# Performance work log

Hardware: AMD Instinct MI355X
Metric: run time of the kernel (lower is better)

## Reference

```python
import jax, jax.numpy as jnp
import numpy as np

# Model dims (match init_kwargs)
HID = 1024   # hidden_size
H   = 16     # num_heads
DK  = 64     # head_dim (key)
DV  = 128    # head value dim = int(head_dim * expand_v)
VAL = H * DV # value_dim = 2048
CONV = 4     # short conv kernel size
EPS = 1e-6
NORM_EPS = 1e-5


def _causal_conv_silu(x, w):
    # x: [B,T,C], w: [C,K] depthwise causal conv, no bias, silu activation
    T = x.shape[1]
    K = w.shape[1]
    xp = jnp.pad(x, ((0, 0), (K - 1, 0), (0, 0)))
    y = sum(xp[:, i:i + T, :] * w[:, i] for i in range(K))
    return jax.nn.silu(y)


def setup_inputs() -> dict:
    key = jax.random.key(0)
    ks = jax.random.split(key, 16)
    s = 0.02
    rn = lambda k, sh: jax.random.normal(k, sh, jnp.float32)
    return {
        'hidden_states': rn(ks[0], (1, 2048, HID)),
        'norm_w': jnp.ones((HID,), jnp.float32),
        'q_w': rn(ks[1], (H * DK, HID)) * s,
        'k_w': rn(ks[2], (H * DK, HID)) * s,
        'v_w': rn(ks[3], (VAL, HID)) * s,
        'a_w': rn(ks[4], (H, HID)) * s,
        'b_w': rn(ks[5], (H, HID)) * s,
        'g_w': rn(ks[6], (VAL, HID)) * s,
        'dt_bias': jax.random.uniform(ks[7], (H,), jnp.float32, -2.0, 0.0),
        'A_log': jnp.log(jax.random.uniform(ks[8], (H,), jnp.float32, 1.0, 8.0)),
        'conv_q_w': rn(ks[9], (H * DK, CONV)) * 0.2,
        'conv_k_w': rn(ks[10], (H * DK, CONV)) * 0.2,
        'conv_v_w': rn(ks[11], (VAL, CONV)) * 0.2,
        'o_norm_w': jnp.ones((DV,), jnp.float32),
        'o_proj_w': rn(ks[12], (HID, VAL)) * s,
        'out_proj_w': rn(ks[13], (HID, HID)) * s,
    }


def reference(hidden_states, norm_w, q_w, k_w, v_w, a_w, b_w, g_w, dt_bias,
              A_log, conv_q_w, conv_k_w, conv_v_w, o_norm_w, o_proj_w, out_proj_w):
    B, T, D = hidden_states.shape
    # RMSNorm
    x = hidden_states * jax.lax.rsqrt(
        jnp.mean(hidden_states * hidden_states, -1, keepdims=True) + EPS) * norm_w

    # projections + causal depthwise short conv + silu
    q = _causal_conv_silu(x @ q_w.T, conv_q_w).reshape(B, T, H, DK)
    k = _causal_conv_silu(x @ k_w.T, conv_k_w).reshape(B, T, H, DK)
    v = _causal_conv_silu(x @ v_w.T, conv_v_w).reshape(B, T, H, DV)

    beta = jax.nn.sigmoid(x @ b_w.T)                       # [B,T,H]
    g = -jnp.exp(A_log) * jax.nn.softplus(x @ a_w.T + dt_bias)  # [B,T,H] log-decay

    # rank-1 DC removal on keys: (I - 1 1^T / DK) k, i.e. subtract per-head mean
    k = k - jnp.mean(k, -1, keepdims=True)

    # L2 normalize q, k along head dim; scale q
    q = q * jax.lax.rsqrt(jnp.sum(q * q, -1, keepdims=True) + EPS)
    k = k * jax.lax.rsqrt(jnp.sum(k * k, -1, keepdims=True) + EPS)
    q = q * (DK ** -0.5)

    # gated delta-rule recurrence over time (time-major scan)
    qT = q.transpose(1, 0, 2, 3)
    kT = k.transpose(1, 0, 2, 3)
    vT = v.transpose(1, 0, 2, 3)
    bT = beta.transpose(1, 0, 2)
    gT = g.transpose(1, 0, 2)

    def step(S, inp):
        qt, kt, vt, bt, gt = inp              # S: [B,H,DK,DV]
        S = S * jnp.exp(gt)[..., None, None]
        v_new = (vt - jnp.einsum('bhk,bhkv->bhv', kt, S)) * bt[..., None]
        S = S + jnp.einsum('bhk,bhv->bhkv', kt, v_new)
        o = jnp.einsum('bhk,bhkv->bhv', qt, S)
        return S, o

    S0 = jnp.zeros((B, H, DK, DV), x.dtype)
    _, oT = jax.lax.scan(step, S0, (qT, kT, vT, bT, gT))
    o = oT.transpose(1, 0, 2, 3)                           # [B,T,H,DV]

    # gated RMSNorm on output heads
    gate = (x @ g_w.T).reshape(B, T, H, DV)
    o = o * jax.lax.rsqrt(jnp.mean(o * o, -1, keepdims=True) + NORM_EPS) * o_norm_w
    o = o * jax.nn.silu(gate)

    o = o.reshape(B, T, VAL) @ o_proj_w.T                  # [B,T,HID]
    return o @ out_proj_w.T
```

## Files before the change

kernel.cpp:

```cpp
#include <hip/hip_runtime.h>
#include <math.h>

#define S72 72

typedef __bf16 bf16;
typedef __bf16 bf16x8 __attribute__((ext_vector_type(8)));
typedef __bf16 bf16x4v __attribute__((ext_vector_type(4)));
typedef __bf16 bf16x2v __attribute__((ext_vector_type(2)));
typedef float f32x4 __attribute__((ext_vector_type(4)));

__device__ __forceinline__ float wredsum(float v) {
#pragma unroll
  for (int off = 32; off > 0; off >>= 1) v += __shfl_xor(v, off, 64);
  return v;
}
__device__ __forceinline__ float sigmoidf_(float x) { return 1.f / (1.f + __expf(-x)); }

__device__ __forceinline__ int sxy(int row, int col) {
  return (row << 6) + ((((col >> 3) ^ (row & 7)) << 3) | (col & 7));
}
__device__ __forceinline__ int sx8(int row, int chunk) {
  return (row << 6) + ((chunk ^ (row & 7)) << 3);
}

__global__ __launch_bounds__(256) void k_pre(const float* __restrict__ h,
    const float* __restrict__ nw, const float* __restrict__ aw,
    const float* __restrict__ bw, const float* __restrict__ dtb,
    const float* __restrict__ alog, bf16* __restrict__ xb,
    float* __restrict__ graw, float* __restrict__ btb,
    const float* __restrict__ qw, const float* __restrict__ kw,
    const float* __restrict__ vw, const float* __restrict__ gw,
    const float* __restrict__ opw, const float* __restrict__ ow,
    bf16* qwb, bf16* kwb, bf16* vwb, bf16* gwb, bf16* opwb, bf16* owb) {
  __shared__ float red[4];
  __shared__ __align__(16) float xs[1024];
  int tid = threadIdx.x;
  if (blockIdx.x >= 2048) {
    long cb = blockIdx.x - 2048;
    for (long u = cb*256 + tid; u < 2359296; u += 4608l*256) {
      const float* src; bf16* dst; long l;
      if      (u <  262144) { src=qw;  dst=qwb;  l=u; }
      else if (u <  524288) { src=kw;  dst=kwb;  l=u-262144; }
      else if (u < 1048576) { src=vw;  dst=vwb;  l=u-524288; }
      else if (u < 1572864) { src=gw;  dst=gwb;  l=u-1048576; }
      else if (u < 2097152) { src=opw; dst=opwb; l=u-1572864; }
      else                  { src=ow;  dst=owb;  l=u-2097152; }
      float4 s = *(const float4*)(src + l*4);
      bf16x4v b; b[0]=(bf16)s.x; b[1]=(bf16)s.y; b[2]=(bf16)s.z; b[3]=(bf16)s.w;
      *(bf16x4v*)(dst + l*4) = b;
    }
    return;
  }
  int t = blockIdx.x;
  float4 hv = *(const float4*)(h + (size_t)t*1024 + tid*4);
  float ss = hv.x*hv.x + hv.y*hv.y + hv.z*hv.z + hv.w*hv.w;
  float wsum = wredsum(ss);
  if ((tid & 63) == 0) red[tid >> 6] = wsum;
  __syncthreads();
  float tot = red[0] + red[1] + red[2] + red[3];
  float rs = rsqrtf(tot * (1.f/1024.f) + 1e-6f);
  float4 w4 = *(const float4*)(nw + tid*4);
  float4 y;
  y.x = hv.x*rs*w4.x; y.y = hv.y*rs*w4.y; y.z = hv.z*rs*w4.z; y.w = hv.w*rs*w4.w;
  *(float4*)(xs + tid*4) = y;
  bf16x4v b; b[0]=(bf16)y.x; b[1]=(bf16)y.y; b[2]=(bf16)y.z; b[3]=(bf16)y.w;
  *(bf16x4v*)(xb + (size_t)t*1024 + tid*4) = b;
  __syncthreads();
  int wave = tid >> 6, lane = tid & 63;
  const float4* x4 = (const float4*)xs;
#pragma unroll
  for (int hi = 0; hi < 4; ++hi) {
    int hh = wave*4 + hi;
    float sa = 0.f, sb = 0.f;
#pragma unroll
    for (int i = 0; i < 4; ++i) {
      float4 xv = x4[i*64 + lane];
      float4 av = *(const float4*)(aw + hh*1024 + i*256 + lane*4);
      float4 bv = *(const float4*)(bw + hh*1024 + i*256 + lane*4);
      sa += xv.x*av.x + xv.y*av.y + xv.z*av.z + xv.w*av.w;
      sb += xv.x*bv.x + xv.y*bv.y + xv.z*bv.z + xv.w*bv.w;
    }
    sa = wredsum(sa); sb = wredsum(sb);
    if (lane == 0) {
      float ap = sa + dtb[hh];
      float sp = (ap > 20.f) ? ap : log1pf(expf(ap));
      graw[t*16 + hh] = -expf(alog[hh]) * sp;
      btb[t*16 + hh] = 1.f / (1.f + expf(-sb));
    }
  }
}

template <typename OutT>
__device__ __forceinline__ void gemm_body(const bf16* __restrict__ A,
    const bf16* __restrict__ B, OutT* __restrict__ C, int N, int K, int m0, int n0) {
  __shared__ bf16 As[2][128*32];
  __shared__ bf16 Bs[2][128*32];
  const int tid = threadIdx.x, lane = tid & 63, wave = tid >> 6;
  const int wm = (wave >> 1) * 64, wn = (wave & 1) * 64;
  const int srow = wave*16 + (lane >> 2);
  const int swl = (((lane & 3) ^ ((lane >> 3) & 3))) * 8;
  const int sdst = (lane & 3) * 8;
  const int quad = lane >> 4, l16 = lane & 15;
  const int sw = (l16 >> 1) & 3;
  f32x4 acc[4][4] = {};
  const int nk = K >> 5;
#pragma unroll
  for (int i = 0; i < 2; ++i) {
    int r = i*64 + srow;
    __builtin_amdgcn_global_load_lds(
      (__attribute__((address_space(1))) void*)(A + (size_t)(m0 + r)*K + swl),
      (__attribute__((address_space(3))) void*)(&As[0][r*32 + sdst]), 16, 0, 0);
    __builtin_amdgcn_global_load_lds(
      (__attribute__((address_space(1))) void*)(B + (size_t)(n0 + r)*K + swl),
      (__attribute__((address_space(3))) void*)(&Bs[0][r*32 + sdst]), 16, 0, 0);
  }
  for (int kt = 0; kt < nk; ++kt) {
    const int cur = kt & 1;
    __syncthreads();
    bf16x8 af[4], bfr[4];
#pragma unroll
    for (int mt = 0; mt < 4; ++mt)
      af[mt] = *(const bf16x8*)(&As[cur][(wm + mt*16 + l16)*32 + (quad ^ sw)*8]);
#pragma unroll
    for (int nt = 0; nt < 4; ++nt)
      bfr[nt] = *(const bf16x8*)(&Bs[cur][(wn + nt*16 + l16)*32 + (quad ^ sw)*8]);
    if (kt + 1 < nk) {
      int k0 = (kt + 1) << 5;
#pragma unroll
      for (int i = 0; i < 2; ++i) {
        int r = i*64 + srow;
        __builtin_amdgcn_global_load_lds(
          (__attribute__((address_space(1))) void*)(A + (size_t)(m0 + r)*K + k0 + swl),
          (__attribute__((address_space(3))) void*)(&As[cur^1][r*32 + sdst]), 16, 0, 0);
        __builtin_amdgcn_global_load_lds(
          (__attribute__((address_space(1))) void*)(B + (size_t)(n0 + r)*K + k0 + swl),
          (__attribute__((address_space(3))) void*)(&Bs[cur^1][r*32 + sdst]), 16, 0, 0);
      }
    }
#pragma unroll
    for (int mt = 0; mt < 4; ++mt)
#pragma unroll
      for (int nt = 0; nt < 4; ++nt)
        acc[mt][nt] = __builtin_amdgcn_mfma_f32_16x16x32_bf16(af[mt], bfr[nt], acc[mt][nt], 0, 0, 0);
  }
#pragma unroll
  for (int mt = 0; mt < 4; ++mt)
#pragma unroll
    for (int nt = 0; nt < 4; ++nt)
#pragma unroll
      for (int r = 0; r < 4; ++r) {
        int row = m0 + wm + mt*16 + quad*4 + r;
        int col = n0 + wn + nt*16 + l16;
        C[(size_t)row*N + col] = (OutT)acc[mt][nt][r];
      }
}

__global__ __launch_bounds__(256) void k_gemm_proj(const bf16* __restrict__ A,
    const bf16* __restrict__ qwb, const bf16* __restrict__ kwb,
    const bf16* __restrict__ vwb, const bf16* __restrict__ gwb,
    bf16* __restrict__ qpre, bf16* __restrict__ kpre,
    bf16* __restrict__ vpre, bf16* __restrict__ gpre) {
  int bx = blockIdx.x;
  const bf16* B; bf16* C; int N, xt;
  if      (bx <  8) { B = qwb; C = qpre; N = 1024; xt = bx; }
  else if (bx < 16) { B = kwb; C = kpre; N = 1024; xt = bx - 8; }
  else if (bx < 32) { B = vwb; C = vpre; N = 2048; xt = bx - 16; }
  else              { B = gwb; C = gpre; N = 2048; xt = bx - 32; }
  gemm_body<bf16>(A, B, C, N, 1024, blockIdx.y*128, xt*128);
}

template <typename OutT>
__global__ __launch_bounds__(256) void k_gemm_bt64(const bf16* __restrict__ A,
    const bf16* __restrict__ B, OutT* __restrict__ C, int N, int K) {
  __shared__ bf16 As[2][128*32];
  __shared__ bf16 Bs[2][64*32];
  const int tid = threadIdx.x, lane = tid & 63, wave = tid >> 6;
  const int wm = wave * 32;
  const int srow = wave*16 + (lane >> 2);
  const int swl = (((lane & 3) ^ ((lane >> 3) & 3))) * 8;
  const int sdst = (lane & 3) * 8;
  const int quad = lane >> 4, l16 = lane & 15;
  const int sw = (l16 >> 1) & 3;
  const int m0 = blockIdx.y * 128, n0 = blockIdx.x * 64;
  f32x4 acc[2][4] = {};
  const int nk = K >> 5;
#pragma unroll
  for (int i = 0; i < 2; ++i) {
    int r = i*64 + srow;
    __builtin_amdgcn_global_load_lds(
      (__attribute__((address_space(1))) void*)(A + (size_t)(m0 + r)*K + swl),
      (__attribute__((address_space(3))) void*)(&As[0][r*32 + sdst]), 16, 0, 0);
  }
  __builtin_amdgcn_global_load_lds(
    (__attribute__((address_space(1))) void*)(B + (size_t)(n0 + srow)*K + swl),
    (__attribute__((address_space(3))) void*)(&Bs[0][srow*32 + sdst]), 16, 0, 0);
  for (int kt = 0; kt < nk; ++kt) {
    const int cur = kt & 1;
    __syncthreads();
    bf16x8 af[2], bfr[4];
#pragma unroll
    for (int mt = 0; mt < 2; ++mt)
      af[mt] = *(const bf16x8*)(&As[cur][(wm + mt*16 + l16)*32 + (quad ^ sw)*8]);
#pragma unroll
    for (int nt = 0; nt < 4; ++nt)
      bfr[nt] = *(const bf16x8*)(&Bs[cur][(nt*16 + l16)*32 + (quad ^ sw)*8]);
    if (kt + 1 < nk) {
      int k0 = (kt + 1) << 5;
#pragma unroll
      for (int i = 0; i < 2; ++i) {
        int r = i*64 + srow;
        __builtin_amdgcn_global_load_lds(
          (__attribute__((address_space(1))) void*)(A + (size_t)(m0 + r)*K + k0 + swl),
          (__attribute__((address_space(3))) void*)(&As[cur^1][r*32 + sdst]), 16, 0, 0);
      }
      __builtin_amdgcn_global_load_lds(
        (__attribute__((address_space(1))) void*)(B + (size_t)(n0 + srow)*K + k0 + swl),
        (__attribute__((address_space(3))) void*)(&Bs[cur^1][srow*32 + sdst]), 16, 0, 0);
    }
#pragma unroll
    for (int mt = 0; mt < 2; ++mt)
#pragma unroll
      for (int nt = 0; nt < 4; ++nt)
        acc[mt][nt] = __builtin_amdgcn_mfma_f32_16x16x32_bf16(af[mt], bfr[nt], acc[mt][nt], 0, 0, 0);
  }
#pragma unroll
  for (int mt = 0; mt < 2; ++mt)
#pragma unroll
    for (int nt = 0; nt < 4; ++nt)
#pragma unroll
      for (int r = 0; r < 4; ++r) {
        int row = m0 + wm + mt*16 + quad*4 + r;
        int col = n0 + nt*16 + l16;
        C[(size_t)row*N + col] = (OutT)acc[mt][nt][r];
      }
}

template<int NT>
__device__ __forceinline__ void mm_band(const bf16* A_lds, const bf16* B_lds,
    int w16, int cb, int l16, int quad, f32x4* acc) {
#pragma unroll
  for (int n = 0; n < NT; ++n) { acc[n][0]=0.f; acc[n][1]=0.f; acc[n][2]=0.f; acc[n][3]=0.f; }
#pragma unroll
  for (int kt = 0; kt < 2; ++kt) {
    bf16x8 af = *(const bf16x8*)(A_lds + sx8(w16 + l16, kt*4 + quad));
#pragma unroll
    for (int n = 0; n < NT; ++n) {
      bf16x8 bf = *(const bf16x8*)(B_lds + sx8(cb + n*16 + l16, kt*4 + quad));
      acc[n] = __builtin_amdgcn_mfma_f32_16x16x32_bf16(af, bf, acc[n], 0, 0, 0);
    }
  }
}

__global__ __launch_bounds__(512, 4) void k_prepass(
    const bf16* __restrict__ qpre, const bf16* __restrict__ kpre,
    const bf16* __restrict__ vpre, const float* __restrict__ cqw,
    const float* __restrict__ ckw, const float* __restrict__ cvw,
    const float* __restrict__ graw, const float* __restrict__ beta,
    bf16* __restrict__ EF, float* __restrict__ dSl, float* __restrict__ obuf) {
  const int bx = blockIdx.x, c = bx >> 4, h = bx & 15, tid = threadIdx.x;
  const int t0 = c * 64;
  const int wave = tid >> 6, lane = tid & 63, l16 = lane & 15, quad = lane >> 4;
  const int w16 = (wave >> 1) * 16;
  const int chh = wave & 1;
  const int r0 = wave * 8;

  __shared__ bf16 SM[36864];
  __shared__ float bs[64], bts_s[64], es[64], gms[64];
  bf16* Kr    = SM;
  bf16* powR0 = SM + 4096;
  bf16* prod0 = SM + 8192;
  bf16* T2T   = SM + 12288;
  bf16* powT0 = SM + 16384;
  bf16* powR1 = SM + 20480;
  bf16* powT1 = SM + 24576;
  bf16* prod1 = SM + 28672;
  bf16* qbf   = SM + 32768;
  bf16* VT   = SM;
  bf16* VlT  = SM + 8192;
  bf16* KT   = powT0;
  bf16* KbT  = powR1;
  bf16* Pm   = powT1;
  bf16* WR   = prod0;
  bf16* Mrow = prod1;

  if (tid < 64) {
    float g = graw[(size_t)(t0 + tid)*16 + h];
    float b = g;
#pragma unroll
    for (int off = 1; off < 64; off <<= 1) {
      float p = __shfl_up(b, off, 64);
      if (tid >= off) b += p;
    }
    bs[tid] = b;
    bts_s[tid] = beta[(size_t)(t0 + tid)*16 + h];
    float b63 = __shfl(b, 63, 64);
    es[tid] = __expf(b63 - b);
    gms[tid] = __expf(b);
  }

  float kreg[8], vreg[16];
  {
    float4 wq  = *(const float4*)(cqw + (h*64 + lane)*4);
    float4 wk  = *(const float4*)(ckw + (h*64 + lane)*4);
    float4 wv0 = *(const float4*)(cvw + (h*128 + lane)*4);
    float4 wv1 = *(const float4*)(cvw + (h*128 + 64 + lane)*4);
    float qtv[11], ktv[11], vtv0[11], vtv1[11];
#pragma unroll
    for (int j = 0; j < 11; ++j) {
      int tg = t0 + r0 + j - 3;
      bool ok = tg >= 0;
      qtv[j]  = ok ? (float)qpre[(size_t)tg*1024 + h*64 + lane] : 0.f;
      ktv[j]  = ok ? (float)kpre[(size_t)tg*1024 + h*64 + lane] : 0.f;
      vtv0[j] = ok ? (float)vpre[(size_t)tg*2048 + h*128 + lane] : 0.f;
      vtv1[j] = ok ? (float)vpre[(size_t)tg*2048 + h*128 + 64 + lane] : 0.f;
    }
#pragma unroll
    for (int rr = 0; rr < 8; ++rr) {
      float y = qtv[rr]*wq.x + qtv[rr+1]*wq.y + qtv[rr+2]*wq.z + qtv[rr+3]*wq.w;
      y = y * sigmoidf_(y);
      float ssq = wredsum(y*y);
      y *= rsqrtf(ssq + 1e-6f) * 0.125f;
      qbf[sxy(r0+rr, lane)] = (bf16)y;
    }
#pragma unroll
    for (int rr = 0; rr < 8; ++rr) {
      float y = ktv[rr]*wk.x + ktv[rr+1]*wk.y + ktv[rr+2]*wk.z + ktv[rr+3]*wk.w;
      y = y * sigmoidf_(y);
      float s1 = y, s2 = y*y;
#pragma unroll
      for (int off = 32; off > 0; off >>= 1) {
        s1 += __shfl_xor(s1, off, 64);
        s2 += __shfl_xor(s2, off, 64);
      }
      float m = s1 * (1.f/64.f);
      float ssq = s2 - s1*m;
      y -= m;
      y *= rsqrtf(ssq + 1e-6f);
      kreg[rr] = y;
      Kr[sxy(r0+rr, lane)] = (bf16)y;
    }
#pragma unroll
    for (int rr = 0; rr < 8; ++rr) {
      float y0 = vtv0[rr]*wv0.x + vtv0[rr+1]*wv0.y + vtv0[rr+2]*wv0.z + vtv0[rr+3]*wv0.w;
      float y1 = vtv1[rr]*wv1.x + vtv1[rr+1]*wv1.y + vtv1[rr+2]*wv1.z + vtv1[rr+3]*wv1.w;
      vreg[rr]   = y0 * sigmoidf_(y0);
      vreg[8+rr] = y1 * sigmoidf_(y1);
    }
  }
  __syncthreads();

  {
    f32x4 acc[2];
    mm_band<2>(Kr, Kr, w16, chh*32, l16, quad, acc);
#pragma unroll
    for (int n = 0; n < 2; ++n) {
      int col = chh*32 + n*16 + l16;
      bf16x4v tv;
#pragma unroll
      for (int r = 0; r < 4; ++r) {
        int row = w16 + quad*4 + r;
        float nv = 0.f;
        if (row > col) nv = -bts_s[row] * __expf(bs[row] - bs[col]) * acc[n][r];
        bf16 nb = (bf16)nv;
        powR0[sxy(row, col)] = nb;
        tv[r] = nb;
        prod0[sxy(row, col)] = (row == col) ? (bf16)1.f : nb;
      }
      *(bf16x4v*)(powT0 + sxy(col, w16 + quad*4)) = tv;
    }
  }
  __syncthreads();

  int pc = 0, rc = 0;
#pragma unroll 1
  for (int i = 1; i <= 5; ++i) {
    bf16* sqA = pc ? powR1 : powR0;
    bf16* sqB = pc ? powT1 : powT0;
    bf16* sqRo = pc ? powR0 : powR1;
    bf16* sqTo = pc ? powT0 : powT1;
    {
      f32x4 acc[2];
      mm_band<2>(sqA, sqB, w16, chh*32, l16, quad, acc);
#pragma unroll
      for (int n = 0; n < 2; ++n) {
        int col = chh*32 + n*16 + l16;
        bf16x4v tv;
#pragma unroll
        for (int r = 0; r < 4; ++r) {
          int row = w16 + quad*4 + r;
          bf16 vb = (bf16)acc[n][r];
          sqRo[sxy(row, col)] = vb;
          tv[r] = vb;
        }
        *(bf16x4v*)(sqTo + sxy(col, w16 + quad*4)) = tv;
      }
    }
    __syncthreads();
    bf16* prA = rc ? prod1 : prod0;
    bf16* prO = rc ? prod0 : prod1;
    {
      f32x4 acc[2];
      mm_band<2>(prA, sqTo, w16, chh*32, l16, quad, acc);
#pragma unroll
      for (int n = 0; n < 2; ++n) {
        int col = chh*32 + n*16 + l16;
        bf16x4v tv;
#pragma unroll
        for (int r = 0; r < 4; ++r) {
          int row = w16 + quad*4 + r;
          float val = acc[n][r] + (float)prA[sxy(row, col)];
          prO[sxy(row, col)] = (bf16)val;
          tv[r] = (bf16)(val * bts_s[col] * gms[col]);
        }
        if (i == 5) *(bf16x4v*)(T2T + sxy(col, w16 + quad*4)) = tv;
      }
    }
    __syncthreads();
    pc ^= 1; rc ^= 1;
  }

#pragma unroll
  for (int rr = 0; rr < 8; ++rr) {
    KT[sxy(lane, r0+rr)]  = (bf16)kreg[rr];
    KbT[sxy(lane, r0+rr)] = (bf16)(kreg[rr] * es[r0+rr]);
  }
  {
    f32x4 acc[2];
#pragma unroll
    for (int n = 0; n < 2; ++n) { acc[n][0]=0.f; acc[n][1]=0.f; acc[n][2]=0.f; acc[n][3]=0.f; }
#pragma unroll
    for (int kt = 0; kt < 2; ++kt) {
      bf16x8 af = *(const bf16x8*)(qbf + sx8(w16 + l16, kt*4 + quad));
#pragma unroll
      for (int n = 0; n < 2; ++n) {
        bf16x8 bf = *(const bf16x8*)(Kr + sx8(chh*32 + n*16 + l16, kt*4 + quad));
        acc[n] = __builtin_amdgcn_mfma_f32_16x16x32_bf16(af, bf, acc[n], 0, 0, 0);
      }
    }
#pragma unroll
    for (int n = 0; n < 2; ++n) {
      int col = chh*32 + n*16 + l16;
#pragma unroll
      for (int r = 0; r < 4; ++r) {
        int row = w16 + quad*4 + r;
        float pv = (row >= col) ? __expf(bs[row] - bs[col]) * acc[n][r] : 0.f;
        Pm[sxy(row, col)] = (bf16)pv;
      }
    }
  }
  __syncthreads();

  {
    f32x4 acc[2];
    mm_band<2>(KbT, T2T, w16, chh*32, l16, quad, acc);
#pragma unroll
    for (int n = 0; n < 2; ++n) {
      int col = chh*32 + n*16 + l16;
#pragma unroll
      for (int r = 0; r < 4; ++r)
        WR[sxy(w16 + quad*4 + r, col)] = (bf16)acc[n][r];
    }
  }
#pragma unroll
  for (int hf = 0; hf < 2; ++hf)
#pragma unroll
    for (int rr = 0; rr < 8; ++rr)
      VT[sxy(hf*64 + lane, r0+rr)] = (bf16)(bts_s[r0+rr] * vreg[hf*8+rr]);
  __syncthreads();
  {
    f32x4 acc[2];
    mm_band<2>(WR, KT, w16, chh*32, l16, quad, acc);
    float gC = gms[63];
    size_t eb = (size_t)bx * 13824;
#pragma unroll
    for (int n = 0; n < 2; ++n) {
      int col = chh*32 + n*16 + l16;
#pragma unroll
      for (int r = 0; r < 4; ++r) {
        int row = w16 + quad*4 + r;
        float ev = ((row == col) ? gC : 0.f) - acc[n][r];
        bf16 eh = (bf16)ev;
        EF[eb + row*S72 + col] = eh;
        EF[eb + 4608 + row*S72 + col] = (bf16)(ev - (float)eh);
      }
    }
  }
  __syncthreads();
  {
    f32x4 acc[2];
    mm_band<2>(Pm, T2T, w16, chh*32, l16, quad, acc);
#pragma unroll
    for (int n = 0; n < 2; ++n) {
      int col = chh*32 + n*16 + l16;
#pragma unroll
      for (int r = 0; r < 4; ++r)
        WR[sxy(w16 + quad*4 + r, col)] = (bf16)acc[n][r];
    }
  }
  __syncthreads();
  {
    f32x4 acc[2];
    mm_band<2>(WR, KT, w16, chh*32, l16, quad, acc);
    size_t eb = (size_t)bx * 13824;
#pragma unroll
    for (int n = 0; n < 2; ++n) {
      int col = chh*32 + n*16 + l16;
#pragma unroll
      for (int r = 0; r < 4; ++r) {
        int row = w16 + quad*4 + r;
        float qv = (float)qbf[sxy(row, col)];
        EF[eb + 9216 + row*S72 + col] = (bf16)(gms[row]*qv - acc[n][r]);
      }
    }
  }
  __syncthreads();
  {
    f32x4 acc[4];
    mm_band<4>(Mrow, VT, w16, chh*64, l16, quad, acc);
#pragma unroll
    for (int n = 0; n < 4; ++n) {
      int col = chh*64 + n*16 + l16;
      bf16x4v tv;
#pragma unroll
      for (int r = 0; r < 4; ++r) tv[r] = (bf16)acc[n][r];
      *(bf16x4v*)(VlT + sxy(col, w16 + quad*4)) = tv;
    }
  }
  __syncthreads();
  {
    f32x4 acc[4];
    mm_band<4>(KbT, VlT, w16, chh*64, l16, quad, acc);
#pragma unroll
    for (int n = 0; n < 4; ++n) {
      int col = chh*64 + n*16 + l16;
#pragma unroll
      for (int r = 0; r < 4; ++r)
        dSl[(size_t)bx*8192 + (size_t)(w16 + quad*4 + r)*128 + col] = acc[n][r];
    }
  }
  {
    f32x4 acc[4];
    mm_band<4>(Pm, VlT, w16, chh*64, l16, quad, acc);
#pragma unroll
    for (int n = 0; n < 4; ++n) {
      int col = chh*64 + n*16 + l16;
#pragma unroll
      for (int r = 0; r < 4; ++r)
        obuf[(size_t)(t0 + w16 + quad*4 + r)*2048 + h*128 + col] = acc[n][r];
    }
  }
}

#define SEQ_LOAD(Cn, EHx, ELx, FFx, DSx)                                        \
  {                                                                             \
    const bf16* base_ = EF + (size_t)((Cn)*16 + h)*13824 + arow;                \
    _Pragma("unroll")                                                           \
    for (int kt = 0; kt < 2; ++kt) {                                            \
      EHx[kt] = *(const bf16x8*)(base_ + kt*32);                                \
      ELx[kt] = *(const bf16x8*)(base_ + 4608 + kt*32);                         \
      FFx[kt] = *(const bf16x8*)(base_ + 9216 + kt*32);                         \
    }                                                                           \
    const float* db_ = dSl + (size_t)((Cn)*16 + h)*8192 + drow;                 \
    _Pragma("unroll")                                                           \
    for (int nt = 0; nt < 2; ++nt)                                              \
      _Pragma("unroll")                                                         \
      for (int r = 0; r < 4; ++r)                                               \
        DSx[nt*4+r] = db_[(size_t)r*128 + nt*16];                               \
  }

#define SEQ_STEP(Cc, EHc, ELc, FFc, DSc, EHn, ELn, FFn, DSn, SRC, DST)          \
  {                                                                             \
    bf16x8 bh[2][2], bl[2][2];                                                  \
    _Pragma("unroll")                                                           \
    for (int nt = 0; nt < 2; ++nt)                                              \
      _Pragma("unroll")                                                         \
      for (int kt = 0; kt < 2; ++kt) {                                          \
        bh[nt][kt] = *(const bf16x8*)(&Sthi[SRC][(nt*16 + l16)*S72 + kt*32 + quad*8]); \
        bl[nt][kt] = *(const bf16x8*)(&Stlo[SRC][(nt*16 + l16)*S72 + kt*32 + quad*8]); \
      }                                                                         \
    if ((Cc) + 1 < 32) SEQ_LOAD((Cc) + 1, EHn, ELn, FFn, DSn);                  \
    f32x4 a1[2], a2[2], a3[2], o1[2], o2[2];                                    \
    _Pragma("unroll")                                                           \
    for (int nt = 0; nt < 2; ++nt)                                              \
      _Pragma("unroll")                                                         \
      for (int r = 0; r < 4; ++r) {                                             \
        a1[nt][r] = DSc[nt*4+r];                                                \
        a2[nt][r] = 0.f; a3[nt][r] = 0.f; o1[nt][r] = 0.f; o2[nt][r] = 0.f;     \
      }                                                                         \
    _Pragma("unroll")                                                           \
    for (int kt = 0; kt < 2; ++kt)                                              \
      _Pragma("unroll")                                                         \
      for (int nt = 0; nt < 2; ++nt) {                                          \
        a1[nt] = __builtin_amdgcn_mfma_f32_16x16x32_bf16(EHc[kt], bh[nt][kt], a1[nt], 0, 0, 0); \
        a2[nt] = __builtin_amdgcn_mfma_f32_16x16x32_bf16(EHc[kt], bl[nt][kt], a2[nt], 0, 0, 0); \
        a3[nt] = __builtin_amdgcn_mfma_f32_16x16x32_bf16(ELc[kt], bh[nt][kt], a3[nt], 0, 0, 0); \
        o1[nt] = __builtin_amdgcn_mfma_f32_16x16x32_bf16(FFc[kt], bh[nt][kt], o1[nt], 0, 0, 0); \
        o2[nt] = __builtin_amdgcn_mfma_f32_16x16x32_bf16(FFc[kt], bl[nt][kt], o2[nt], 0, 0, 0); \
      }                                                                         \
    {                                                                           \
      int t0c = (Cc)*64;                                                        \
      _Pragma("unroll")                                                         \
      for (int nt = 0; nt < 2; ++nt)                                            \
        _Pragma("unroll")                                                       \
        for (int r = 0; r < 4; ++r)                                             \
          osb[(size_t)(t0c + mb + quad*4 + r)*2048 + h*128 + dq*32 + nt*16 + l16] \
            = o1[nt][r] + o2[nt][r];                                            \
    }                                                                           \
    _Pragma("unroll")                                                           \
    for (int nt = 0; nt < 2; ++nt) {                                            \
      bf16x4v hv, lv;                                                           \
      _Pragma("unroll")                                                         \
      for (int r = 0; r < 4; ++r) {                                             \
        float v = a1[nt][r] + a2[nt][r] + a3[nt][r];                            \
        bf16 hb = (bf16)v;                                                      \
        hv[r] = hb;                                                             \
        lv[r] = (bf16)(v - (float)hb);                                          \
      }                                                                         \
      *(bf16x4v*)(&Sthi[DST][(nt*16 + l16)*S72 + mb + quad*4]) = hv;            \
      *(bf16x4v*)(&Stlo[DST][(nt*16 + l16)*S72 + mb + quad*4]) = lv;            \
    }                                                                           \
    asm volatile("s_waitcnt lgkmcnt(0)" ::: "memory");                          \
    __builtin_amdgcn_s_barrier();                                               \
  }

__global__ __launch_bounds__(256) void k_seq(const bf16* __restrict__ EF,
    const float* __restrict__ dSl, float* __restrict__ osb) {
  const int bid = blockIdx.x;
  const int h = (bid & 7) + 8*((bid >> 3) & 1);
  const int dq = bid >> 4;
  const int tid = threadIdx.x, wave = tid >> 6, lane = tid & 63;
  const int l16 = lane & 15, quad = lane >> 4;
  const int mb = wave * 16;
  __shared__ bf16 Sthi[2][32*S72], Stlo[2][32*S72];
  for (int i = tid; i < 2304; i += 256) { Sthi[0][i] = (bf16)0.f; Stlo[0][i] = (bf16)0.f; }

  const size_t arow = (size_t)(mb + l16)*S72 + quad*8;
  const size_t drow = (size_t)dq*32 + (size_t)(mb + quad*4)*128 + l16;

  bf16x8 ehA[2], elA[2], ffA[2], ehB[2], elB[2], ffB[2];
  float dsA[8], dsB[8];

  SEQ_LOAD(0, ehA, elA, ffA, dsA);
  asm volatile("s_waitcnt lgkmcnt(0)" ::: "memory");
  __builtin_amdgcn_s_barrier();

#pragma unroll 1
  for (int c = 0; c < 32; c += 2) {
    SEQ_STEP(c,     ehA, elA, ffA, dsA, ehB, elB, ffB, dsB, 0, 1);
    SEQ_STEP(c + 1, ehB, elB, ffB, dsB, ehA, elA, ffA, dsA, 1, 0);
  }
}

__global__ __launch_bounds__(256) void k_gatenorm(const float* __restrict__ o,
    const float* __restrict__ os, const bf16* __restrict__ gpre,
    const float* __restrict__ onw, bf16* __restrict__ og) {
  int t = blockIdx.x, wave = threadIdx.x >> 6, lane = threadIdx.x & 63;
  float2 nw = *(const float2*)(onw + lane*2);
#pragma unroll
  for (int hi = 0; hi < 4; ++hi) {
    int hh = wave*4 + hi;
    size_t base = (size_t)t*2048 + hh*128 + lane*2;
    float2 o2 = *(const float2*)(o + base);
    float2 s2 = *(const float2*)(os + base);
    o2.x += s2.x; o2.y += s2.y;
    float ss = wredsum(o2.x*o2.x + o2.y*o2.y);
    float rs = rsqrtf(ss * (1.f/128.f) + 1e-5f);
    bf16x2v g2 = *(const bf16x2v*)(gpre + base);
    float g0 = (float)g2[0], g1 = (float)g2[1];
    float r0 = o2.x * rs * nw.x * (g0 * sigmoidf_(g0));
    float r1 = o2.y * rs * nw.y * (g1 * sigmoidf_(g1));
    bf16x2v b; b[0] = (bf16)r0; b[1] = (bf16)r1;
    *(bf16x2v*)(og + base) = b;
  }
}

extern "C" void kernel_launch(void* const* d_in, const int* in_sizes, int n_in,
                              void* d_out, int out_size, void* d_ws, size_t ws_size,
                              hipStream_t stream) {
  const float* hs   = (const float*)d_in[0];
  const float* nw   = (const float*)d_in[1];
  const float* qw   = (const float*)d_in[2];
  const float* kw   = (const float*)d_in[3];
  const float* vw   = (const float*)d_in[4];
  const float* aw   = (const float*)d_in[5];
  const float* bw   = (const float*)d_in[6];
  const float* gw   = (const float*)d_in[7];
  const float* dtb  = (const float*)d_in[8];
  const float* alog = (const float*)d_in[9];
  const float* cqw  = (const float*)d_in[10];
  const float* ckw  = (const float*)d_in[11];
  const float* cvw  = (const float*)d_in[12];
  const float* onw  = (const float*)d_in[13];
  const float* opw  = (const float*)d_in[14];
  const float* ow   = (const float*)d_in[15];
  float* out = (float*)d_out;

  char* p = (char*)d_ws;
  auto alloc = [&](size_t bytes) { char* r = p; p += (bytes + 255) & ~255ull; return r; };
  bf16*  xb    = (bf16*) alloc((size_t)2048*1024*2);
  bf16*  qwb   = (bf16*) alloc((size_t)1024*1024*2);
  bf16*  kwb   = (bf16*) alloc((size_t)1024*1024*2);
  bf16*  vwb   = (bf16*) alloc((size_t)2048*1024*2);
  bf16*  gwb   = (bf16*) alloc((size_t)2048*1024*2);
  bf16*  opwb  = (bf16*) alloc((size_t)1024*2048*2);
  bf16*  owb   = (bf16*) alloc((size_t)1024*1024*2);
  bf16*  qpre  = (bf16*) alloc((size_t)2048*1024*2);
  bf16*  kpre  = (bf16*) alloc((size_t)2048*1024*2);
  bf16*  vpre  = (bf16*) alloc((size_t)2048*2048*2);
  bf16*  gpre  = (bf16*) alloc((size_t)2048*2048*2);
  float* graw  = (float*)alloc((size_t)2048*16*4);
  float* btb   = (float*)alloc((size_t)2048*16*4);
  float* ob    = (float*)alloc((size_t)2048*2048*4);
  bf16*  ogb   = (bf16*) alloc((size_t)2048*2048*2);
  bf16*  h1b   = (bf16*) alloc((size_t)2048*1024*2);
  bf16*  EF    = (bf16*) alloc((size_t)512*13824*2);
  float* osb   = (float*)alloc((size_t)512*8192*4);
  float* dSl   = (float*)xb;

  k_pre<<<2048+4608, 256, 0, stream>>>(hs, nw, aw, bw, dtb, alog, xb, graw, btb,
                                       qw, kw, vw, gw, opw, ow,
                                       qwb, kwb, vwb, gwb, opwb, owb);
  k_gemm_proj<<<dim3(48,16,1), 256, 0, stream>>>(xb, qwb, kwb, vwb, gwb, qpre, kpre, vpre, gpre);
  k_prepass<<<512, 512, 0, stream>>>(qpre, kpre, vpre, cqw, ckw, cvw, graw, btb, EF, dSl, ob);
  k_seq<<<64, 256, 0, stream>>>(EF, dSl, osb);
  k_gatenorm<<<2048, 256, 0, stream>>>(ob, osb, gpre, onw, ogb);
  k_gemm_bt64<bf16><<<dim3(16,16,1), 256, 0, stream>>>(ogb, opwb, h1b, 1024, 2048);
  k_gemm_bt64<float><<<dim3(16,16,1), 256, 0, stream>>>(h1b, owb, out, 1024, 1024);
}
```

Measured before the change: 271.6 us.

## Software-pipeline Neumann power/product phases in prepass to cut barriers

```diff
diff --git a/kernel.cpp b/kernel.cpp
--- a/kernel.cpp
+++ b/kernel.cpp
@@ -251,6 +251,45 @@
   }
 }
 
+__device__ __forceinline__ void sq_phase(const bf16* Sr, const bf16* St,
+    bf16* Ro, bf16* To, int w16, int chh, int l16, int quad) {
+  f32x4 acc[2];
+  mm_band<2>(Sr, St, w16, chh*32, l16, quad, acc);
+#pragma unroll
+  for (int n = 0; n < 2; ++n) {
+    int col = chh*32 + n*16 + l16;
+    bf16x4v tv;
+#pragma unroll
+    for (int r = 0; r < 4; ++r) {
+      int row = w16 + quad*4 + r;
+      bf16 vb = (bf16)acc[n][r];
+      Ro[sxy(row, col)] = vb;
+      tv[r] = vb;
+    }
+    *(bf16x4v*)(To + sxy(col, w16 + quad*4)) = tv;
+  }
+}
+
+__device__ __forceinline__ void prod_phase(const bf16* Pr, const bf16* St, bf16* Po,
+    bf16* T2o, const float* bts_s, const float* gms,
+    int w16, int chh, int l16, int quad) {
+  f32x4 acc[2];
+  mm_band<2>(Pr, St, w16, chh*32, l16, quad, acc);
+#pragma unroll
+  for (int n = 0; n < 2; ++n) {
+    int col = chh*32 + n*16 + l16;
+    bf16x4v tv;
+#pragma unroll
+    for (int r = 0; r < 4; ++r) {
+      int row = w16 + quad*4 + r;
+      float val = acc[n][r] + (float)Pr[sxy(row, col)];
+      Po[sxy(row, col)] = (bf16)val;
+      tv[r] = (bf16)(val * bts_s[col] * gms[col]);
+    }
+    if (T2o) *(bf16x4v*)(T2o + sxy(col, w16 + quad*4)) = tv;
+  }
+}
+
 __global__ __launch_bounds__(512, 4) void k_prepass(
     const bf16* __restrict__ qpre, const bf16* __restrict__ kpre,
     const bf16* __restrict__ vpre, const float* __restrict__ cqw,
@@ -266,22 +305,17 @@
 
   __shared__ bf16 SM[36864];
   __shared__ float bs[64], bts_s[64], es[64], gms[64];
-  bf16* Kr    = SM;
-  bf16* powR0 = SM + 4096;
-  bf16* prod0 = SM + 8192;
-  bf16* T2T   = SM + 12288;
-  bf16* powT0 = SM + 16384;
-  bf16* powR1 = SM + 20480;
-  bf16* powT1 = SM + 24576;
-  bf16* prod1 = SM + 28672;
-  bf16* qbf   = SM + 32768;
-  bf16* VT   = SM;
-  bf16* VlT  = SM + 8192;
-  bf16* KT   = powT0;
-  bf16* KbT  = powR1;
-  bf16* Pm   = powT1;
-  bf16* WR   = prod0;
-  bf16* Mrow = prod1;
+  bf16* pA = SM;
+  bf16* pB = SM + 4096;
+  bf16* pC = SM + 8192;
+  bf16* pD = SM + 12288;
+  bf16* pE = SM + 16384;
+  bf16* pF = SM + 20480;
+  bf16* pG = SM + 24576;
+  bf16* pH = SM + 28672;
+  bf16* pQ = SM + 32768;
+  bf16* VTb  = SM + 4096;
+  bf16* VlTb = SM + 12288;
 
   if (tid < 64) {
     float g = graw[(size_t)(t0 + tid)*16 + h];
@@ -320,7 +354,7 @@
       y = y * sigmoidf_(y);
       float ssq = wredsum(y*y);
       y *= rsqrtf(ssq + 1e-6f) * 0.125f;
-      qbf[sxy(r0+rr, lane)] = (bf16)y;
+      pQ[sxy(r0+rr, lane)] = (bf16)y;
     }
 #pragma unroll
     for (int rr = 0; rr < 8; ++rr) {
@@ -337,7 +371,7 @@
       y -= m;
       y *= rsqrtf(ssq + 1e-6f);
       kreg[rr] = y;
-      Kr[sxy(r0+rr, lane)] = (bf16)y;
+      pA[sxy(r0+rr, lane)] = (bf16)y;
     }
 #pragma unroll
     for (int rr = 0; rr < 8; ++rr) {
@@ -351,7 +385,7 @@
 
   {
     f32x4 acc[2];
-    mm_band<2>(Kr, Kr, w16, chh*32, l16, quad, acc);
+    mm_band<2>(pA, pA, w16, chh*32, l16, quad, acc);
 #pragma unroll
     for (int n = 0; n < 2; ++n) {
       int col = chh*32 + n*16 + l16;
@@ -362,78 +396,57 @@
         float nv = 0.f;
         if (row > col) nv = -bts_s[row] * __expf(bs[row] - bs[col]) * acc[n][r];
         bf16 nb = (bf16)nv;
-        powR0[sxy(row, col)] = nb;
+        pB[sxy(row, col)] = nb;
         tv[r] = nb;
-        prod0[sxy(row, col)] = (row == col) ? (bf16)1.f : nb;
-      }
-      *(bf16x4v*)(powT0 + sxy(col, w16 + quad*4)) = tv;
-    }
-  }
-  __syncthreads();
-
-  int pc = 0, rc = 0;
-#pragma unroll 1
-  for (int i = 1; i <= 5; ++i) {
-    bf16* sqA = pc ? powR1 : powR0;
-    bf16* sqB = pc ? powT1 : powT0;
-    bf16* sqRo = pc ? powR0 : powR1;
-    bf16* sqTo = pc ? powT0 : powT1;
-    {
-      f32x4 acc[2];
-      mm_band<2>(sqA, sqB, w16, chh*32, l16, quad, acc);
+        pC[sxy(row, col)] = (row == col) ? (bf16)1.f : nb;
+      }
+      *(bf16x4v*)(pE + sxy(col, w16 + quad*4)) = tv;
+    }
+  }
+  __syncthreads();
+
+  sq_phase(pB, pE, pF, pG, w16, chh, l16, quad);
+  __syncthreads();
+  sq_phase(pF, pG, pB, pE, w16, chh, l16, quad);
+  prod_phase(pC, pG, pH, nullptr, bts_s, gms, w16, chh, l16, quad);
+  __syncthreads();
+  sq_phase(pB, pE, pF, pG, w16, chh, l16, quad);
+  prod_phase(pH, pE, pC, nullptr, bts_s, gms, w16, chh, l16, quad);
+  __syncthreads();
+  sq_phase(pF, pG, pB, pE, w16, chh, l16, quad);
+  prod_phase(pC, pG, pH, nullptr, bts_s, gms, w16, chh, l16, quad);
+  __syncthreads();
+  {
+    f32x4 acc[2];
+    mm_band<2>(pB, pE, w16, chh*32, l16, quad, acc);
+#pragma unroll
+    for (int n = 0; n < 2; ++n) {
+      int col = chh*32 + n*16 + l16;
+      bf16x4v tv;
+#pragma unroll
+      for (int r = 0; r < 4; ++r) tv[r] = (bf16)acc[n][r];
+      *(bf16x4v*)(pG + sxy(col, w16 + quad*4)) = tv;
+    }
+  }
+  prod_phase(pH, pE, pC, nullptr, bts_s, gms, w16, chh, l16, quad);
+  __syncthreads();
+  prod_phase(pC, pG, pH, pD, bts_s, gms, w16, chh, l16, quad);
+#pragma unroll
+  for (int rr = 0; rr < 8; ++rr) {
+    pE[sxy(lane, r0+rr)] = (bf16)kreg[rr];
+    pF[sxy(lane, r0+rr)] = (bf16)(kreg[rr] * es[r0+rr]);
+  }
+  __syncthreads();
+  {
+    f32x4 acc[2];
+#pragma unroll
+    for (int n = 0; n < 2; ++n) { acc[n][0]=0.f; acc[n][1]=0.f; acc[n][2]=0.f; acc[n][3]=0.f; }
+#pragma unroll
+    for (int kt = 0; kt < 2; ++kt) {
+      bf16x8 af = *(const bf16x8*)(pQ + sx8(w16 + l16, kt*4 + quad));
 #pragma unroll
       for (int n = 0; n < 2; ++n) {
-        int col = chh*32 + n*16 + l16;
-        bf16x4v tv;
-#pragma unroll
-        for (int r = 0; r < 4; ++r) {
-          int row = w16 + quad*4 + r;
-          bf16 vb = (bf16)acc[n][r];
-          sqRo[sxy(row, col)] = vb;
-          tv[r] = vb;
-        }
-        *(bf16x4v*)(sqTo + sxy(col, w16 + quad*4)) = tv;
-      }
-    }
-    __syncthreads();
-    bf16* prA = rc ? prod1 : prod0;
-    bf16* prO = rc ? prod0 : prod1;
-    {
-      f32x4 acc[2];
-      mm_band<2>(prA, sqTo, w16, chh*32, l16, quad, acc);
-#pragma unroll
-      for (int n = 0; n < 2; ++n) {
-        int col = chh*32 + n*16 + l16;
-        bf16x4v tv;
-#pragma unroll
-        for (int r = 0; r < 4; ++r) {
-          int row = w16 + quad*4 + r;
-          float val = acc[n][r] + (float)prA[sxy(row, col)];
-          prO[sxy(row, col)] = (bf16)val;
-          tv[r] = (bf16)(val * bts_s[col] * gms[col]);
-        }
-        if (i == 5) *(bf16x4v*)(T2T + sxy(col, w16 + quad*4)) = tv;
-      }
-    }
-    __syncthreads();
-    pc ^= 1; rc ^= 1;
-  }
-
-#pragma unroll
-  for (int rr = 0; rr < 8; ++rr) {
-    KT[sxy(lane, r0+rr)]  = (bf16)kreg[rr];
-    KbT[sxy(lane, r0+rr)] = (bf16)(kreg[rr] * es[r0+rr]);
-  }
-  {
-    f32x4 acc[2];
-#pragma unroll
-    for (int n = 0; n < 2; ++n) { acc[n][0]=0.f; acc[n][1]=0.f; acc[n][2]=0.f; acc[n][3]=0.f; }
-#pragma unroll
-    for (int kt = 0; kt < 2; ++kt) {
-      bf16x8 af = *(const bf16x8*)(qbf + sx8(w16 + l16, kt*4 + quad));
-#pragma unroll
-      for (int n = 0; n < 2; ++n) {
-        bf16x8 bf = *(const bf16x8*)(Kr + sx8(chh*32 + n*16 + l16, kt*4 + quad));
+        bf16x8 bf = *(const bf16x8*)(pA + sx8(chh*32 + n*16 + l16, kt*4 + quad));
         acc[n] = __builtin_amdgcn_mfma_f32_16x16x32_bf16(af, bf, acc[n], 0, 0, 0);
       }
     }
@@ -444,32 +457,25 @@
       for (int r = 0; r < 4; ++r) {
         int row = w16 + quad*4 + r;
         float pv = (row >= col) ? __expf(bs[row] - bs[col]) * acc[n][r] : 0.f;
-        Pm[sxy(row, col)] = (bf16)pv;
-      }
-    }
-  }
-  __syncthreads();
-
+        pG[sxy(row, col)] = (bf16)pv;
+      }
+    }
+  }
   {
     f32x4 acc[2];
-    mm_band<2>(KbT, T2T, w16, chh*32, l16, quad, acc);
+    mm_band<2>(pF, pD, w16, chh*32, l16, quad, acc);
 #pragma unroll
     for (int n = 0; n < 2; ++n) {
       int col = chh*32 + n*16 + l16;
 #pragma unroll
       for (int r = 0; r < 4; ++r)
-        WR[sxy(w16 + quad*4 + r, col)] = (bf16)acc[n][r];
-    }
-  }
-#pragma unroll
-  for (int hf = 0; hf < 2; ++hf)
-#pragma unroll
-    for (int rr = 0; rr < 8; ++rr)
-      VT[sxy(hf*64 + lane, r0+rr)] = (bf16)(bts_s[r0+rr] * vreg[hf*8+rr]);
+        pC[sxy(w16 + quad*4 + r, col)] = (bf16)acc[n][r];
+    }
+  }
   __syncthreads();
   {
     f32x4 acc[2];
-    mm_band<2>(WR, KT, w16, chh*32, l16, quad, acc);
+    mm_band<2>(pC, pE, w16, chh*32, l16, quad, acc);
     float gC = gms[63];
     size_t eb = (size_t)bx * 13824;
 #pragma unroll
@@ -485,22 +491,21 @@
       }
     }
   }
-  __syncthreads();
   {
     f32x4 acc[2];
-    mm_band<2>(Pm, T2T, w16, chh*32, l16, quad, acc);
+    mm_band<2>(pG, pD, w16, chh*32, l16, quad, acc);
 #pragma unroll
     for (int n = 0; n < 2; ++n) {
       int col = chh*32 + n*16 + l16;
 #pragma unroll
       for (int r = 0; r < 4; ++r)
-        WR[sxy(w16 + quad*4 + r, col)] = (bf16)acc[n][r];
+        pA[sxy(w16 + quad*4 + r, col)] = (bf16)acc[n][r];
     }
   }
   __syncthreads();
   {
     f32x4 acc[2];
-    mm_band<2>(WR, KT, w16, chh*32, l16, quad, acc);
+    mm_band<2>(pA, pE, w16, chh*32, l16, quad, acc);
     size_t eb = (size_t)bx * 13824;
 #pragma unroll
     for (int n = 0; n < 2; ++n) {
@@ -508,28 +513,33 @@
 #pragma unroll
       for (int r = 0; r < 4; ++r) {
         int row = w16 + quad*4 + r;
-        float qv = (float)qbf[sxy(row, col)];
+        float qv = (float)pQ[sxy(row, col)];
         EF[eb + 9216 + row*S72 + col] = (bf16)(gms[row]*qv - acc[n][r]);
       }
     }
   }
+#pragma unroll
+  for (int hf = 0; hf < 2; ++hf)
+#pragma unroll
+    for (int rr = 0; rr < 8; ++rr)
+      VTb[sxy(hf*64 + lane, r0+rr)] = (bf16)(bts_s[r0+rr] * vreg[hf*8+rr]);
   __syncthreads();
   {
     f32x4 acc[4];
-    mm_band<4>(Mrow, VT, w16, chh*64, l16, quad, acc);
+    mm_band<4>(pH, VTb, w16, chh*64, l16, quad, acc);
 #pragma unroll
     for (int n = 0; n < 4; ++n) {
       int col = chh*64 + n*16 + l16;
       bf16x4v tv;
 #pragma unroll
       for (int r = 0; r < 4; ++r) tv[r] = (bf16)acc[n][r];
-      *(bf16x4v*)(VlT + sxy(col, w16 + quad*4)) = tv;
+      *(bf16x4v*)(VlTb + sxy(col, w16 + quad*4)) = tv;
     }
   }
   __syncthreads();
   {
     f32x4 acc[4];
-    mm_band<4>(KbT, VlT, w16, chh*64, l16, quad, acc);
+    mm_band<4>(pF, VlTb, w16, chh*64, l16, quad, acc);
 #pragma unroll
     for (int n = 0; n < 4; ++n) {
       int col = chh*64 + n*16 + l16;
@@ -540,7 +550,7 @@
   }
   {
     f32x4 acc[4];
-    mm_band<4>(Pm, VlT, w16, chh*64, l16, quad, acc);
+    mm_band<4>(pG, VlTb, w16, chh*64, l16, quad, acc);
 #pragma unroll
     for (int n = 0; n < 4; ++n) {
       int col = chh*64 + n*16 + l16;
```

Measured after the change: 270.2 us. About the same (-0.5%).
